# Optimization experiments

Measured on AMD Instinct MI355X. Metric: run time of the kernel, lower is better.

Reference implementation:

```python
import jax, jax.numpy as jnp
import numpy as np

LENGTH, D, CHI, CLASSES = 784, 2, 128, 10
BATCH = 1024


def setup_inputs() -> dict:
    key = jax.random.key(0)
    k1, k2, k3 = jax.random.split(key, 3)
    # feature-mapped samples (batch, d, length), values in [0,1] like cossin map
    x = jax.random.uniform(k1, (BATCH, D, LENGTH), dtype=jnp.float32)
    # per-site residual weights; small init so the residual recurrence stays stable
    W = jax.random.normal(k2, (LENGTH, D, CHI, CHI), dtype=jnp.float32) * (0.01 / np.sqrt(CHI))
    # classifier matrix applied to the final hidden vector
    V = jax.random.normal(k3, (CHI, CLASSES), dtype=jnp.float32) / np.sqrt(CHI)
    return {"x": x, "W": W, "V": V}


def reference(x, W, V):
    # x: (B, d, L), W: (L, d, chi, chi), V: (chi, classes)
    B = x.shape[0]
    chi = W.shape[2]
    h0 = jnp.ones((B, chi), dtype=x.dtype)  # initial hidden bond vector

    xs = jnp.moveaxis(x, 2, 0)  # (L, B, d) so scan iterates over sites

    def site_step(h, inputs):
        xn, Wn = inputs  # xn: (B, d), Wn: (d, chi, chi)
        # residual MPS update: h <- h + sum_{s,a} x[n,s] W_n[s,a,b] h[a]
        h = h + jnp.einsum('ns,sab,na->nb', xn, Wn, h)
        return h, None

    h, _ = jax.lax.scan(site_step, h0, (xs, W))
    logits = h @ V  # (B, classes)
    return logits
```

## Files before the change

kernel.cpp:

```cpp
#include <hip/hip_runtime.h>

#define LL 784
#define CHI 128
#define CLS 10
#define BC 16
#define NBLK 64

typedef __attribute__((ext_vector_type(8))) short short8;
typedef __attribute__((ext_vector_type(4))) float floatx4;

__device__ inline unsigned int f2bf(float v) {
    unsigned int u = __float_as_uint(v);
    u += 0x7fffu + ((u >> 16) & 1u);
    return u >> 16;
}

__device__ inline void lds_barrier() {
    asm volatile("s_waitcnt lgkmcnt(0)\n\ts_barrier" ::: "memory");
}

__device__ inline unsigned int cvt_pk_bf16(float lo, float hi) {
    unsigned int r;
    asm("v_cvt_pk_bf16_f32 %0, %1, %2" : "=v"(r) : "v"(lo), "v"(hi));
    return r;
}

__global__ __launch_bounds__(256) void prep_kernel(const float* __restrict__ W,
                                                   uint4* __restrict__ ws4) {
    __shared__ float tile[32 * 132];
    const int b = blockIdx.x;
    const int n = b >> 3, s = (b >> 2) & 1, kt = b & 3;
    const float* Wp = W + ((size_t)(n * 2 + s) * CHI + kt * 32) * CHI;
    const int t = threadIdx.x;
    #pragma unroll
    for (int k = 0; k < 4; k++) {
        int v = t + k * 256;
        int a = v >> 5, c4 = v & 31;
        float4 val = *(const float4*)(Wp + a * CHI + c4 * 4);
        *(float4*)&tile[a * 132 + c4 * 4] = val;
    }
    __syncthreads();
    const int l = t & 63, f0 = t >> 6;
    const int m_ = l & 15, q_ = l >> 4;
    #pragma unroll
    for (int ff = 0; ff < 2; ff++) {
        int nt = f0 + ff * 4;
        const float* tp = &tile[(q_ * 8) * 132 + nt * 16 + m_];
        uint4 pk;
        pk.x = f2bf(tp[0 * 132]) | (f2bf(tp[1 * 132]) << 16);
        pk.y = f2bf(tp[2 * 132]) | (f2bf(tp[3 * 132]) << 16);
        pk.z = f2bf(tp[4 * 132]) | (f2bf(tp[5 * 132]) << 16);
        pk.w = f2bf(tp[6 * 132]) | (f2bf(tp[7 * 132]) << 16);
        ws4[(size_t)(((n * 8 + nt) * 2 + s) * 4 + kt) * 64 + l] = pk;
    }
}

__global__ __launch_bounds__(256, 1) void mps_kernel(const float* __restrict__ x,
                                                     const unsigned short* __restrict__ ws,
                                                     const float* __restrict__ V,
                                                     float* __restrict__ out) {
    __shared__ short8 bfbuf[2][4][64];
    __shared__ float hfin[BC * 136];

    const int t = threadIdx.x;
    const int w = t >> 6, l = t & 63;
    const int m = l & 15, q = l >> 4;
    const int rb = blockIdx.x * BC;

    for (int i = t; i < 1024; i += 256)
        ((unsigned int*)&bfbuf[0][0][0])[i] = 0x3F803F80u;

    const float* xp0 = x + (size_t)(rb + m) * (2 * LL);
    const float* xp1 = xp0 + LL;
    float4 xA0, xA1, xA2, xA3, xB0, xB1, xB2, xB3;
    xA0 = *(const float4*)(xp0 + 0);  xA1 = *(const float4*)(xp0 + 4);
    xA2 = *(const float4*)(xp1 + 0);  xA3 = *(const float4*)(xp1 + 4);

    const unsigned short* wsw = ws + (size_t)w * 8192 + (size_t)l * 8;
    short8 bWA[16], bWB[16];
    #pragma unroll
    for (int f = 0; f < 16; f++) {
        bWA[f] = *(const short8*)(wsw + (size_t)0 * 32768 + f * 512);
        bWB[f] = *(const short8*)(wsw + (size_t)1 * 32768 + f * 512);
    }

    floatx4 hacc0 = (floatx4){1.f, 1.f, 1.f, 1.f};
    floatx4 hacc1 = (floatx4){1.f, 1.f, 1.f, 1.f};

    unsigned int* const bfw = (unsigned int*)&bfbuf[0][0][0];
    const int wr_dw = w * 256 + (q >> 1) * 64 + m * 4 + (q & 1) * 2;

#define SITE_BODY(NN, PAR, WBUF, X0, X1) do {                                       \
    lds_barrier();                                                                  \
    short8 bf0 = bfbuf[PAR][0][l];                                                  \
    short8 bf1 = bfbuf[PAR][1][l];                                                  \
    short8 bf2 = bfbuf[PAR][2][l];                                                  \
    short8 bf3 = bfbuf[PAR][3][l];                                                  \
    floatx4 z = (floatx4){0.f, 0.f, 0.f, 0.f};                                      \
    floatx4 p0l = __builtin_amdgcn_mfma_f32_16x16x32_bf16(WBUF[0],  bf0, z, 0,0,0); \
    floatx4 p0h = __builtin_amdgcn_mfma_f32_16x16x32_bf16(WBUF[2],  bf2, z, 0,0,0); \
    floatx4 p1l = __builtin_amdgcn_mfma_f32_16x16x32_bf16(WBUF[4],  bf0, z, 0,0,0); \
    floatx4 p1h = __builtin_amdgcn_mfma_f32_16x16x32_bf16(WBUF[6],  bf2, z, 0,0,0); \
    floatx4 q0l = __builtin_amdgcn_mfma_f32_16x16x32_bf16(WBUF[8],  bf0, z, 0,0,0); \
    floatx4 q0h = __builtin_amdgcn_mfma_f32_16x16x32_bf16(WBUF[10], bf2, z, 0,0,0); \
    floatx4 q1l = __builtin_amdgcn_mfma_f32_16x16x32_bf16(WBUF[12], bf0, z, 0,0,0); \
    floatx4 q1h = __builtin_amdgcn_mfma_f32_16x16x32_bf16(WBUF[14], bf2, z, 0,0,0); \
    p0l = __builtin_amdgcn_mfma_f32_16x16x32_bf16(WBUF[1],  bf1, p0l, 0,0,0);       \
    p0h = __builtin_amdgcn_mfma_f32_16x16x32_bf16(WBUF[3],  bf3, p0h, 0,0,0);       \
    p1l = __builtin_amdgcn_mfma_f32_16x16x32_bf16(WBUF[5],  bf1, p1l, 0,0,0);       \
    p1h = __builtin_amdgcn_mfma_f32_16x16x32_bf16(WBUF[7],  bf3, p1h, 0,0,0);       \
    q0l = __builtin_amdgcn_mfma_f32_16x16x32_bf16(WBUF[9],  bf1, q0l, 0,0,0);       \
    q0h = __builtin_amdgcn_mfma_f32_16x16x32_bf16(WBUF[11], bf3, q0h, 0,0,0);       \
    q1l = __builtin_amdgcn_mfma_f32_16x16x32_bf16(WBUF[13], bf1, q1l, 0,0,0);       \
    q1h = __builtin_amdgcn_mfma_f32_16x16x32_bf16(WBUF[15], bf3, q1h, 0,0,0);       \
    if ((NN) + 2 < LL) {                                                            \
        _Pragma("unroll")                                                           \
        for (int f = 0; f < 16; f++)                                                \
            WBUF[f] = *(const short8*)(wsw + (size_t)((NN) + 2) * 32768 + f * 512); \
    }                                                                               \
    _Pragma("unroll")                                                               \
    for (int i = 0; i < 4; i++) {                                                   \
        hacc0[i] += (X0) * (p0l[i] + p0h[i]) + (X1) * (p1l[i] + p1h[i]);            \
        hacc1[i] += (X0) * (q0l[i] + q0h[i]) + (X1) * (q1l[i] + q1h[i]);            \
    }                                                                               \
    uint2 pk0, pk1;                                                                 \
    pk0.x = cvt_pk_bf16(hacc0[0], hacc0[1]);                                        \
    pk0.y = cvt_pk_bf16(hacc0[2], hacc0[3]);                                        \
    pk1.x = cvt_pk_bf16(hacc1[0], hacc1[1]);                                        \
    pk1.y = cvt_pk_bf16(hacc1[2], hacc1[3]);                                        \
    *(uint2*)&bfw[((PAR) ^ 1) * 1024 + wr_dw]       = pk0;                          \
    *(uint2*)&bfw[((PAR) ^ 1) * 1024 + 128 + wr_dw] = pk1;                          \
} while (0)

    for (int nb = 0; nb < LL; nb += 16) {
        if (nb + 8 < LL) {
            xB0 = *(const float4*)(xp0 + nb + 8);
            xB1 = *(const float4*)(xp0 + nb + 12);
            xB2 = *(const float4*)(xp1 + nb + 8);
            xB3 = *(const float4*)(xp1 + nb + 12);
        }
        SITE_BODY(nb + 0,  0, bWA, xA0.x, xA2.x);
        SITE_BODY(nb + 1,  1, bWB, xA0.y, xA2.y);
        SITE_BODY(nb + 2,  0, bWA, xA0.z, xA2.z);
        SITE_BODY(nb + 3,  1, bWB, xA0.w, xA2.w);
        SITE_BODY(nb + 4,  0, bWA, xA1.x, xA3.x);
        SITE_BODY(nb + 5,  1, bWB, xA1.y, xA3.y);
        SITE_BODY(nb + 6,  0, bWA, xA1.z, xA3.z);
        SITE_BODY(nb + 7,  1, bWB, xA1.w, xA3.w);
        if (nb + 16 < LL) {
            xA0 = *(const float4*)(xp0 + nb + 16);
            xA1 = *(const float4*)(xp0 + nb + 20);
            xA2 = *(const float4*)(xp1 + nb + 16);
            xA3 = *(const float4*)(xp1 + nb + 20);
        }
        SITE_BODY(nb + 8,  0, bWA, xB0.x, xB2.x);
        SITE_BODY(nb + 9,  1, bWB, xB0.y, xB2.y);
        SITE_BODY(nb + 10, 0, bWA, xB0.z, xB2.z);
        SITE_BODY(nb + 11, 1, bWB, xB0.w, xB2.w);
        SITE_BODY(nb + 12, 0, bWA, xB1.x, xB3.x);
        SITE_BODY(nb + 13, 1, bWB, xB1.y, xB3.y);
        SITE_BODY(nb + 14, 0, bWA, xB1.z, xB3.z);
        SITE_BODY(nb + 15, 1, bWB, xB1.w, xB3.w);
    }
#undef SITE_BODY

    *(floatx4*)&hfin[m * 136 + w * 32 + q * 4]      = hacc0;
    *(floatx4*)&hfin[m * 136 + w * 32 + 16 + q * 4] = hacc1;
    __syncthreads();

    if (t < BC * CLS) {
        int r = t / CLS, cls = t % CLS;
        float sum = 0.f;
        for (int a = 0; a < CHI; a++) sum += hfin[r * 136 + a] * V[a * CLS + cls];
        out[(size_t)(rb + r) * CLS + cls] = sum;
    }
}

extern "C" void kernel_launch(void* const* d_in, const int* in_sizes, int n_in,
                              void* d_out, int out_size, void* d_ws, size_t ws_size,
                              hipStream_t stream) {
    const float* x = (const float*)d_in[0];
    const float* W = (const float*)d_in[1];
    const float* V = (const float*)d_in[2];
    float* out = (float*)d_out;

    prep_kernel<<<LL * 8, 256, 0, stream>>>(W, (uint4*)d_ws);
    mps_kernel<<<NBLK, 256, 0, stream>>>(x, (const unsigned short*)d_ws, V, out);
}
```

Measured before the change: 686.4 us.

## Split hidden-state columns across 8 waves and hand-schedule weight prefetch loads

The recurrent kernel moves from 4 to 8 waves per block, so each wave owns 16 output columns instead of 32 and issues 8 MFMAs per site instead of 16. This halves the per-wave serial work on the latency-bound scan chain. Weight and x loads are now inline-asm global loads with explicit vmcnt waits, which lets the next-site prefetch overlap the current MFMAs. In exchange the block-wide barrier every site now spans 8 waves, and the hand-counted vmcnt(8) waits are fragile if load ordering or counts drift.

```diff
diff --git a/kernel.cpp b/kernel.cpp
--- a/kernel.cpp
+++ b/kernel.cpp
@@ -23,6 +23,30 @@
     unsigned int r;
     asm("v_cvt_pk_bf16_f32 %0, %1, %2" : "=v"(r) : "v"(lo), "v"(hi));
     return r;
+}
+
+template <int OFF>
+__device__ inline short8 gload(const char* p) {
+    short8 r;
+    asm volatile("global_load_dwordx4 %0, %1, off offset:%2"
+                 : "=v"(r) : "v"(p), "i"(OFF));
+    return r;
+}
+
+__device__ inline floatx4 gloadf4(const float* p) {
+    floatx4 r;
+    asm volatile("global_load_dwordx4 %0, %1, off"
+                 : "=v"(r) : "v"(p));
+    return r;
+}
+
+__device__ inline void vm_wait8() {
+    asm volatile("s_waitcnt vmcnt(8)" ::: "memory");
+    __builtin_amdgcn_sched_barrier(0);
+}
+__device__ inline void vm_wait0() {
+    asm volatile("s_waitcnt vmcnt(0)" ::: "memory");
+    __builtin_amdgcn_sched_barrier(0);
 }
 
 __global__ __launch_bounds__(256) void prep_kernel(const float* __restrict__ W,
@@ -55,10 +79,10 @@
     }
 }
 
-__global__ __launch_bounds__(256, 1) void mps_kernel(const float* __restrict__ x,
-                                                     const unsigned short* __restrict__ ws,
-                                                     const float* __restrict__ V,
-                                                     float* __restrict__ out) {
+__global__ __launch_bounds__(512) void mps_kernel(const float* __restrict__ x,
+                                                  const unsigned short* __restrict__ ws,
+                                                  const float* __restrict__ V,
+                                                  float* __restrict__ out) {
     __shared__ short8 bfbuf[2][4][64];
     __shared__ float hfin[BC * 136];
 
@@ -67,105 +91,121 @@
     const int m = l & 15, q = l >> 4;
     const int rb = blockIdx.x * BC;
 
-    for (int i = t; i < 1024; i += 256)
+    for (int i = t; i < 1024; i += 512)
         ((unsigned int*)&bfbuf[0][0][0])[i] = 0x3F803F80u;
 
     const float* xp0 = x + (size_t)(rb + m) * (2 * LL);
     const float* xp1 = xp0 + LL;
-    float4 xA0, xA1, xA2, xA3, xB0, xB1, xB2, xB3;
-    xA0 = *(const float4*)(xp0 + 0);  xA1 = *(const float4*)(xp0 + 4);
-    xA2 = *(const float4*)(xp1 + 0);  xA3 = *(const float4*)(xp1 + 4);
-
-    const unsigned short* wsw = ws + (size_t)w * 8192 + (size_t)l * 8;
-    short8 bWA[16], bWB[16];
-    #pragma unroll
-    for (int f = 0; f < 16; f++) {
-        bWA[f] = *(const short8*)(wsw + (size_t)0 * 32768 + f * 512);
-        bWB[f] = *(const short8*)(wsw + (size_t)1 * 32768 + f * 512);
-    }
-
-    floatx4 hacc0 = (floatx4){1.f, 1.f, 1.f, 1.f};
-    floatx4 hacc1 = (floatx4){1.f, 1.f, 1.f, 1.f};
+    floatx4 xA0, xA1, xA2, xA3, xB0, xB1, xB2, xB3;
+    xA0 = gloadf4(xp0 + 0);  xA1 = gloadf4(xp0 + 4);
+    xA2 = gloadf4(xp1 + 0);  xA3 = gloadf4(xp1 + 4);
+
+    const char* wsb = (const char*)ws + (size_t)w * 8192 + (size_t)l * 16;
+
+    short8 bWA[8], bWB[8];
+    {
+        const char* p0 = wsb;
+        const char* p1 = wsb + 65536;
+        bWA[0] = gload<0>(p0);           bWA[1] = gload<1024>(p0);
+        bWA[2] = gload<2048>(p0);        bWA[3] = gload<3072>(p0);
+        bWA[4] = gload<0>(p0 + 4096);    bWA[5] = gload<1024>(p0 + 4096);
+        bWA[6] = gload<2048>(p0 + 4096); bWA[7] = gload<3072>(p0 + 4096);
+        bWB[0] = gload<0>(p1);           bWB[1] = gload<1024>(p1);
+        bWB[2] = gload<2048>(p1);        bWB[3] = gload<3072>(p1);
+        bWB[4] = gload<0>(p1 + 4096);    bWB[5] = gload<1024>(p1 + 4096);
+        bWB[6] = gload<2048>(p1 + 4096); bWB[7] = gload<3072>(p1 + 4096);
+    }
+
+    floatx4 hacc = (floatx4){1.f, 1.f, 1.f, 1.f};
 
     unsigned int* const bfw = (unsigned int*)&bfbuf[0][0][0];
-    const int wr_dw = w * 256 + (q >> 1) * 64 + m * 4 + (q & 1) * 2;
-
-#define SITE_BODY(NN, PAR, WBUF, X0, X1) do {                                       \
+    const int wr_dw = (w >> 1) * 256 + (m + 16 * ((w & 1) * 2 + (q >> 1))) * 4 + (q & 1) * 2;
+
+    __syncthreads();
+
+#define SITE_BODY(NN, PAR, WBUF, X0, X1, PF, WAIT) do {                             \
     lds_barrier();                                                                  \
     short8 bf0 = bfbuf[PAR][0][l];                                                  \
     short8 bf1 = bfbuf[PAR][1][l];                                                  \
     short8 bf2 = bfbuf[PAR][2][l];                                                  \
     short8 bf3 = bfbuf[PAR][3][l];                                                  \
+    WAIT();                                                                         \
     floatx4 z = (floatx4){0.f, 0.f, 0.f, 0.f};                                      \
-    floatx4 p0l = __builtin_amdgcn_mfma_f32_16x16x32_bf16(WBUF[0],  bf0, z, 0,0,0); \
-    floatx4 p0h = __builtin_amdgcn_mfma_f32_16x16x32_bf16(WBUF[2],  bf2, z, 0,0,0); \
-    floatx4 p1l = __builtin_amdgcn_mfma_f32_16x16x32_bf16(WBUF[4],  bf0, z, 0,0,0); \
-    floatx4 p1h = __builtin_amdgcn_mfma_f32_16x16x32_bf16(WBUF[6],  bf2, z, 0,0,0); \
-    floatx4 q0l = __builtin_amdgcn_mfma_f32_16x16x32_bf16(WBUF[8],  bf0, z, 0,0,0); \
-    floatx4 q0h = __builtin_amdgcn_mfma_f32_16x16x32_bf16(WBUF[10], bf2, z, 0,0,0); \
-    floatx4 q1l = __builtin_amdgcn_mfma_f32_16x16x32_bf16(WBUF[12], bf0, z, 0,0,0); \
-    floatx4 q1h = __builtin_amdgcn_mfma_f32_16x16x32_bf16(WBUF[14], bf2, z, 0,0,0); \
-    p0l = __builtin_amdgcn_mfma_f32_16x16x32_bf16(WBUF[1],  bf1, p0l, 0,0,0);       \
-    p0h = __builtin_amdgcn_mfma_f32_16x16x32_bf16(WBUF[3],  bf3, p0h, 0,0,0);       \
-    p1l = __builtin_amdgcn_mfma_f32_16x16x32_bf16(WBUF[5],  bf1, p1l, 0,0,0);       \
-    p1h = __builtin_amdgcn_mfma_f32_16x16x32_bf16(WBUF[7],  bf3, p1h, 0,0,0);       \
-    q0l = __builtin_amdgcn_mfma_f32_16x16x32_bf16(WBUF[9],  bf1, q0l, 0,0,0);       \
-    q0h = __builtin_amdgcn_mfma_f32_16x16x32_bf16(WBUF[11], bf3, q0h, 0,0,0);       \
-    q1l = __builtin_amdgcn_mfma_f32_16x16x32_bf16(WBUF[13], bf1, q1l, 0,0,0);       \
-    q1h = __builtin_amdgcn_mfma_f32_16x16x32_bf16(WBUF[15], bf3, q1h, 0,0,0);       \
-    if ((NN) + 2 < LL) {                                                            \
-        _Pragma("unroll")                                                           \
-        for (int f = 0; f < 16; f++)                                                \
-            WBUF[f] = *(const short8*)(wsw + (size_t)((NN) + 2) * 32768 + f * 512); \
+    floatx4 p0 = __builtin_amdgcn_mfma_f32_16x16x32_bf16(WBUF[0], bf0, z, 0, 0, 0); \
+    floatx4 p1 = __builtin_amdgcn_mfma_f32_16x16x32_bf16(WBUF[2], bf2, z, 0, 0, 0); \
+    floatx4 q0 = __builtin_amdgcn_mfma_f32_16x16x32_bf16(WBUF[4], bf0, z, 0, 0, 0); \
+    floatx4 q1 = __builtin_amdgcn_mfma_f32_16x16x32_bf16(WBUF[6], bf2, z, 0, 0, 0); \
+    p0 = __builtin_amdgcn_mfma_f32_16x16x32_bf16(WBUF[1], bf1, p0, 0, 0, 0);        \
+    p1 = __builtin_amdgcn_mfma_f32_16x16x32_bf16(WBUF[3], bf3, p1, 0, 0, 0);        \
+    q0 = __builtin_amdgcn_mfma_f32_16x16x32_bf16(WBUF[5], bf1, q0, 0, 0, 0);        \
+    q1 = __builtin_amdgcn_mfma_f32_16x16x32_bf16(WBUF[7], bf3, q1, 0, 0, 0);        \
+    if (PF) {                                                                       \
+        const char* pb_ = wsb + (size_t)((NN) + 2) * 65536;                         \
+        WBUF[0] = gload<0>(pb_);        WBUF[1] = gload<1024>(pb_);                 \
+        WBUF[2] = gload<2048>(pb_);     WBUF[3] = gload<3072>(pb_);                 \
+        const char* pc_ = pb_ + 4096;                                               \
+        WBUF[4] = gload<0>(pc_);        WBUF[5] = gload<1024>(pc_);                 \
+        WBUF[6] = gload<2048>(pc_);     WBUF[7] = gload<3072>(pc_);                 \
     }                                                                               \
     _Pragma("unroll")                                                               \
-    for (int i = 0; i < 4; i++) {                                                   \
-        hacc0[i] += (X0) * (p0l[i] + p0h[i]) + (X1) * (p1l[i] + p1h[i]);            \
-        hacc1[i] += (X0) * (q0l[i] + q0h[i]) + (X1) * (q1l[i] + q1h[i]);            \
-    }                                                                               \
-    uint2 pk0, pk1;                                                                 \
-    pk0.x = cvt_pk_bf16(hacc0[0], hacc0[1]);                                        \
-    pk0.y = cvt_pk_bf16(hacc0[2], hacc0[3]);                                        \
-    pk1.x = cvt_pk_bf16(hacc1[0], hacc1[1]);                                        \
-    pk1.y = cvt_pk_bf16(hacc1[2], hacc1[3]);                                        \
-    *(uint2*)&bfw[((PAR) ^ 1) * 1024 + wr_dw]       = pk0;                          \
-    *(uint2*)&bfw[((PAR) ^ 1) * 1024 + 128 + wr_dw] = pk1;                          \
+    for (int i = 0; i < 4; i++)                                                     \
+        hacc[i] += (X0) * (p0[i] + p1[i]) + (X1) * (q0[i] + q1[i]);                 \
+    uint2 pk;                                                                       \
+    pk.x = cvt_pk_bf16(hacc[0], hacc[1]);                                           \
+    pk.y = cvt_pk_bf16(hacc[2], hacc[3]);                                           \
+    *(uint2*)&bfw[((PAR) ^ 1) * 1024 + wr_dw] = pk;                                 \
 } while (0)
 
-    for (int nb = 0; nb < LL; nb += 16) {
-        if (nb + 8 < LL) {
-            xB0 = *(const float4*)(xp0 + nb + 8);
-            xB1 = *(const float4*)(xp0 + nb + 12);
-            xB2 = *(const float4*)(xp1 + nb + 8);
-            xB3 = *(const float4*)(xp1 + nb + 12);
-        }
-        SITE_BODY(nb + 0,  0, bWA, xA0.x, xA2.x);
-        SITE_BODY(nb + 1,  1, bWB, xA0.y, xA2.y);
-        SITE_BODY(nb + 2,  0, bWA, xA0.z, xA2.z);
-        SITE_BODY(nb + 3,  1, bWB, xA0.w, xA2.w);
-        SITE_BODY(nb + 4,  0, bWA, xA1.x, xA3.x);
-        SITE_BODY(nb + 5,  1, bWB, xA1.y, xA3.y);
-        SITE_BODY(nb + 6,  0, bWA, xA1.z, xA3.z);
-        SITE_BODY(nb + 7,  1, bWB, xA1.w, xA3.w);
-        if (nb + 16 < LL) {
-            xA0 = *(const float4*)(xp0 + nb + 16);
-            xA1 = *(const float4*)(xp0 + nb + 20);
-            xA2 = *(const float4*)(xp1 + nb + 16);
-            xA3 = *(const float4*)(xp1 + nb + 20);
-        }
-        SITE_BODY(nb + 8,  0, bWA, xB0.x, xB2.x);
-        SITE_BODY(nb + 9,  1, bWB, xB0.y, xB2.y);
-        SITE_BODY(nb + 10, 0, bWA, xB0.z, xB2.z);
-        SITE_BODY(nb + 11, 1, bWB, xB0.w, xB2.w);
-        SITE_BODY(nb + 12, 0, bWA, xB1.x, xB3.x);
-        SITE_BODY(nb + 13, 1, bWB, xB1.y, xB3.y);
-        SITE_BODY(nb + 14, 0, bWA, xB1.z, xB3.z);
-        SITE_BODY(nb + 15, 1, bWB, xB1.w, xB3.w);
-    }
+    for (int nb = 0; nb < LL - 16; nb += 16) {
+        xB0 = gloadf4(xp0 + nb + 8);
+        xB1 = gloadf4(xp0 + nb + 12);
+        xB2 = gloadf4(xp1 + nb + 8);
+        xB3 = gloadf4(xp1 + nb + 12);
+        SITE_BODY(nb + 0,  0, bWA, xA0[0], xA2[0], 1, vm_wait8);
+        SITE_BODY(nb + 1,  1, bWB, xA0[1], xA2[1], 1, vm_wait8);
+        SITE_BODY(nb + 2,  0, bWA, xA0[2], xA2[2], 1, vm_wait8);
+        SITE_BODY(nb + 3,  1, bWB, xA0[3], xA2[3], 1, vm_wait8);
+        SITE_BODY(nb + 4,  0, bWA, xA1[0], xA3[0], 1, vm_wait8);
+        SITE_BODY(nb + 5,  1, bWB, xA1[1], xA3[1], 1, vm_wait8);
+        SITE_BODY(nb + 6,  0, bWA, xA1[2], xA3[2], 1, vm_wait8);
+        SITE_BODY(nb + 7,  1, bWB, xA1[3], xA3[3], 1, vm_wait8);
+        xA0 = gloadf4(xp0 + nb + 16);
+        xA1 = gloadf4(xp0 + nb + 20);
+        xA2 = gloadf4(xp1 + nb + 16);
+        xA3 = gloadf4(xp1 + nb + 20);
+        SITE_BODY(nb + 8,  0, bWA, xB0[0], xB2[0], 1, vm_wait8);
+        SITE_BODY(nb + 9,  1, bWB, xB0[1], xB2[1], 1, vm_wait8);
+        SITE_BODY(nb + 10, 0, bWA, xB0[2], xB2[2], 1, vm_wait8);
+        SITE_BODY(nb + 11, 1, bWB, xB0[3], xB2[3], 1, vm_wait8);
+        SITE_BODY(nb + 12, 0, bWA, xB1[0], xB3[0], 1, vm_wait8);
+        SITE_BODY(nb + 13, 1, bWB, xB1[1], xB3[1], 1, vm_wait8);
+        SITE_BODY(nb + 14, 0, bWA, xB1[2], xB3[2], 1, vm_wait8);
+        SITE_BODY(nb + 15, 1, bWB, xB1[3], xB3[3], 1, vm_wait8);
+    }
+
+    xB0 = gloadf4(xp0 + 768 + 8);
+    xB1 = gloadf4(xp0 + 768 + 12);
+    xB2 = gloadf4(xp1 + 768 + 8);
+    xB3 = gloadf4(xp1 + 768 + 12);
+    SITE_BODY(768, 0, bWA, xA0[0], xA2[0], 1, vm_wait8);
+    SITE_BODY(769, 1, bWB, xA0[1], xA2[1], 1, vm_wait8);
+    SITE_BODY(770, 0, bWA, xA0[2], xA2[2], 1, vm_wait8);
+    SITE_BODY(771, 1, bWB, xA0[3], xA2[3], 1, vm_wait8);
+    SITE_BODY(772, 0, bWA, xA1[0], xA3[0], 1, vm_wait8);
+    SITE_BODY(773, 1, bWB, xA1[1], xA3[1], 1, vm_wait8);
+    SITE_BODY(774, 0, bWA, xA1[2], xA3[2], 1, vm_wait8);
+    SITE_BODY(775, 1, bWB, xA1[3], xA3[3], 1, vm_wait8);
+    SITE_BODY(776, 0, bWA, xB0[0], xB2[0], 1, vm_wait8);
+    SITE_BODY(777, 1, bWB, xB0[1], xB2[1], 1, vm_wait8);
+    SITE_BODY(778, 0, bWA, xB0[2], xB2[2], 1, vm_wait8);
+    SITE_BODY(779, 1, bWB, xB0[3], xB2[3], 1, vm_wait8);
+    SITE_BODY(780, 0, bWA, xB1[0], xB3[0], 1, vm_wait8);
+    SITE_BODY(781, 1, bWB, xB1[1], xB3[1], 1, vm_wait8);
+    SITE_BODY(782, 0, bWA, xB1[2], xB3[2], 0, vm_wait8);
+    SITE_BODY(783, 1, bWB, xB1[3], xB3[3], 0, vm_wait0);
 #undef SITE_BODY
 
-    *(floatx4*)&hfin[m * 136 + w * 32 + q * 4]      = hacc0;
-    *(floatx4*)&hfin[m * 136 + w * 32 + 16 + q * 4] = hacc1;
+    *(floatx4*)&hfin[m * 136 + w * 16 + q * 4] = hacc;
     __syncthreads();
 
     if (t < BC * CLS) {
@@ -185,5 +225,5 @@
     float* out = (float*)d_out;
 
     prep_kernel<<<LL * 8, 256, 0, stream>>>(W, (uint4*)d_ws);
-    mps_kernel<<<NBLK, 256, 0, stream>>>(x, (const unsigned short*)d_ws, V, out);
-}
+    mps_kernel<<<NBLK, 512, 0, stream>>>(x, (const unsigned short*)d_ws, V, out);
+}
```

Result: no change. 684.5 us (-0.3%).
